# Kernel optimization log

Hardware: AMD Instinct MI355X
Metric: run time of the kernel (lower is better)

## Reference

```python
import jax, jax.numpy as jnp
import numpy as np
from jax import lax

# norse default LIF/LI parameters
DT = 0.001
TAU_SYN_INV = 200.0   # 1/5e-3
TAU_MEM_INV = 100.0   # 1/1e-2
V_TH = 1.0
ALPHA = 100.0         # super-spike surrogate slope
SEQ_LEN = 128         # args.sqlen
SCALE = 50.0          # args.scale
HIDDEN = 2048         # args.h2
STATE_DIM = 8         # LunarLander-v2
OUT = 4
BATCH = 256

@jax.custom_vjp
def superspike(x):
    # heaviside forward, SuperSpike surrogate backward
    return (x > 0).astype(x.dtype)

def _ss_fwd(x):
    return superspike(x), x

def _ss_bwd(x, g):
    return (g / (ALPHA * jnp.abs(x) + 1.0) ** 2,)

superspike.defvjp(_ss_fwd, _ss_bwd)

def constant_current_lif_encode(current):
    # current: [B, D]; returns spikes [T, B, D]
    def step(v, _):
        v = v + DT * TAU_MEM_INV * (current - v)  # v_leak = 0
        z = superspike(v - V_TH)
        v = (1.0 - z) * v                          # reset to 0
        return v, z
    _, zs = lax.scan(step, jnp.zeros_like(current), None, length=SEQ_LEN)
    return zs

def setup_inputs() -> dict:
    key = jax.random.key(0)
    k1, k2, k3, k4 = jax.random.split(key, 4)
    x = jax.random.normal(k1, (BATCH, STATE_DIM), dtype=jnp.float32)
    w_in = jax.random.normal(k2, (HIDDEN, 2 * STATE_DIM), dtype=jnp.float32) / np.sqrt(2 * STATE_DIM)
    w_rec = jax.random.normal(k3, (HIDDEN, HIDDEN), dtype=jnp.float32) / np.sqrt(HIDDEN)
    w_out = jax.random.normal(k4, (OUT, HIDDEN), dtype=jnp.float32) / np.sqrt(HIDDEN)
    return {"x": x, "w_in": w_in, "w_rec": w_rec, "w_out": w_out}

def reference(x, w_in, w_rec, w_out):
    # encode positive and negative rectified currents, concat on feature dim
    x_pos = constant_current_lif_encode(jax.nn.relu(SCALE * x))
    x_neg = constant_current_lif_encode(jax.nn.relu(-SCALE * x))
    xs = jnp.concatenate([x_pos, x_neg], axis=2)   # [T, B, 2*D]
    B = x.shape[0]
    H = w_in.shape[0]
    O = w_out.shape[0]
    # precompute feed-forward input currents for all timesteps (batched GEMM)
    cur_in = jnp.einsum('tbi,hi->tbh', xs, w_in)   # [T, B, H]
    def step(carry, c_t):
        z, v, i, vo, io = carry
        # LIF recurrent cell (norse lif_step): decay with old state, spike, reset, then current jump
        v_dec = v + DT * TAU_MEM_INV * (-v + i)
        i_dec = i * (1.0 - DT * TAU_SYN_INV)
        z_new = superspike(v_dec - V_TH)
        v_new = (1.0 - z_new) * v_dec              # v_reset = 0
        i_new = i_dec + c_t + z @ w_rec.T          # recurrent uses previous spikes
        # dropout p=0 (eval) -> identity
        # LI readout (norse li_linear_step): vo updates from old io, then io decays + jumps
        vo_new = vo + DT * TAU_MEM_INV * (-vo + io)
        io_new = io * (1.0 - DT * TAU_SYN_INV) + z_new @ w_out.T
        return (z_new, v_new, i_new, vo_new, io_new), vo_new
    dt = x.dtype
    init = (jnp.zeros((B, H), dt), jnp.zeros((B, H), dt), jnp.zeros((B, H), dt),
            jnp.zeros((B, O), dt), jnp.zeros((B, O), dt))
    _, voltages = lax.scan(step, init, cur_in)     # [T, B, O]
    m = jnp.max(voltages, axis=0)
    return jax.nn.softmax(m, axis=1)
```

## Files before the change

### kernel.cpp

```cpp
#include <hip/hip_runtime.h>
#include <math.h>

#define NB 256
#define NH 2048
#define ND 8
#define NI 16
#define NT 128
#define NO 4
#define KK2 33
#define NTHR 512

typedef __attribute__((ext_vector_type(4))) int i32x4;
typedef __attribute__((ext_vector_type(2))) long i64x2;
typedef __attribute__((ext_vector_type(2))) unsigned u32x2;

#define SSTR     (128u*KK2*1024u)
#define OFF_W4   0u
#define SZ_W4    (4u*SSTR)
#define OFF_SC   (OFF_W4 + SZ_W4)
#define OFF_SCF  (OFF_SC + 8192u)
#define ZBUF_B   (16u*KK2*1024u)
#define OFF_ZB   (OFF_SCF + 8192u)
#define SZ_ZB    (2u*ZBUF_B)
#define OFF_XS   (OFF_ZB + SZ_ZB)
#define SZ_XS    ((unsigned)NT*NB*NI)
#define OFF_V    (OFF_XS + SZ_XS)
#define SZ_V     ((unsigned)NB*NH*4u)
#define OFF_I    (OFF_V + SZ_V)
#define OFF_PIO  (OFF_I + SZ_V)
#define SZ_PIO   (2u*NB*64u*NO*4u)
#define OFF_VIO  (OFF_PIO + SZ_PIO)

__global__ __launch_bounds__(512) void k_scale(const float* __restrict__ w_rec,
                                               const float* __restrict__ w_in,
                                               char* __restrict__ wsb) {
    const int gt = blockIdx.x * 512 + threadIdx.x;
    const int h = gt >> 6, lane = gt & 63;
    float m = 0.0f;
    for (int k = lane; k < NH; k += 64) m = fmaxf(m, fabsf(w_rec[h * NH + k]));
    if (lane < 16) m = fmaxf(m, fabsf(w_in[h * NI + lane]));
    #pragma unroll
    for (int d = 1; d < 64; d <<= 1) m = fmaxf(m, __shfl_xor(m, d, 64));
    if (lane == 0) {
        int e;
        frexpf(m, &e);
        int s = 30 - e;
        ((float*)(wsb + OFF_SCF))[h] = ldexpf(1.0f, s);
        ((float*)(wsb + OFF_SC))[h]  = ldexpf(1.0f, -s);
    }
}

__global__ __launch_bounds__(192) void k_pack(const float* __restrict__ w_rec,
                                              const float* __restrict__ w_in,
                                              char* __restrict__ wsb) {
    const int h = blockIdx.x, c = threadIdx.x;
    if (c >= 132) return;
    const float scale = ((const float*)(wsb + OFF_SCF))[h];
    const int k0 = c * 16;
    const int kk = k0 >> 6, q = (k0 >> 4) & 3;
    unsigned pk[4][4] = {{0u,0u,0u,0u},{0u,0u,0u,0u},{0u,0u,0u,0u},{0u,0u,0u,0u}};
    #pragma unroll
    for (int u = 0; u < 16; ++u) {
        int k = k0 + u;
        float wv = 0.0f;
        if (k < NH) wv = w_rec[h * NH + k];
        else if (k < NH + NI) wv = w_in[h * NI + (k - NH)];
        int wq = __float2int_rn(wv * scale);
        int b0_ = (wq << 24) >> 24;  int r = (wq - b0_) >> 8;
        int b1_ = (r << 24) >> 24;   r = (r - b1_) >> 8;
        int b2_ = (r << 24) >> 24;   int b3_ = (r - b2_) >> 8;
        int bs[4] = {b0_, b1_, b2_, b3_};
        #pragma unroll
        for (int sp = 0; sp < 4; ++sp)
            pk[sp][u >> 2] |= ((unsigned)(unsigned char)bs[sp]) << ((u & 3) * 8);
    }
    char* w4 = wsb + OFF_W4;
    unsigned base = (((unsigned)(h >> 4)) * KK2 + (unsigned)kk) * 1024u
                  + ((unsigned)q * 16u + (unsigned)(h & 15)) * 16u;
    #pragma unroll
    for (int sp = 0; sp < 4; ++sp)
        *(i32x4*)(w4 + (unsigned)sp * SSTR + base) = *(const i32x4*)pk[sp];
}

__global__ __launch_bounds__(256) void k_init(const float* __restrict__ x,
                                              char* __restrict__ wsb) {
    const int g = blockIdx.x * 256 + threadIdx.x;
    unsigned* zb32 = (unsigned*)(wsb + OFF_ZB);
    float* vst = (float*)(wsb + OFF_V);
    float* ist = (float*)(wsb + OFF_I);
    float* vio = (float*)(wsb + OFF_VIO);
    char* xsp = (char*)(wsb + OFF_XS);

    #pragma unroll
    for (int r = 0; r < 5; ++r) {
        unsigned off = (unsigned)g + (unsigned)r * 65536u;
        if (off < (SZ_ZB / 4u)) zb32[off] = 0u;
    }
    #pragma unroll
    for (int r = 0; r < 8; ++r) vst[g + r * 65536] = 0.0f;
    #pragma unroll
    for (int r = 0; r < 8; ++r) ist[g + r * 65536] = 0.0f;
    if (g < 3072) vio[g] = (g < 2048) ? 0.0f : -3.0e38f;

    if (g < NB * NI) {
        const int b = g >> 4, ci = g & 15;
        float xv = x[b * ND + (ci & 7)];
        float c = (ci < 8) ? __fmul_rn(50.0f, xv) : __fmul_rn(-50.0f, xv);
        c = fmaxf(c, 0.0f);
        float ev = 0.0f;
        for (int t = 0; t < NT; ++t) {
            ev = __fadd_rn(ev, __fmul_rn(0.1f, __fsub_rn(c, ev)));
            float z = (__fsub_rn(ev, 1.0f) > 0.0f) ? 1.0f : 0.0f;
            xsp[t * (NB * NI) + g] = (z > 0.0f) ? (char)1 : (char)0;
            ev = (z > 0.0f) ? 0.0f : ev;
        }
    }
}

__global__ __launch_bounds__(256) void k_init2(char* __restrict__ wsb) {
    const int b = threadIdx.x;
    char* zb0 = wsb + OFF_ZB;
    const char* xsp = wsb + OFF_XS;
    i32x4 xv = *(const i32x4*)(xsp + b * 16);
    unsigned dst = (((unsigned)(b >> 4)) * KK2 + 32u) * 1024u + (unsigned)(b & 15) * 16u;
    *(i32x4*)(zb0 + dst) = xv;
}

__global__ __launch_bounds__(NTHR, 2) void k_step(const float* __restrict__ w_out,
                                                  char* __restrict__ wsb, int t) {
    __shared__ float red[4 * 64 * 34];
    __shared__ float z_s[64 * 34];
    __shared__ float w_out_lds[128];

    const int tid = threadIdx.x;
    const int beta = blockIdx.x;
    const int xcd = beta & 7, jb = beta >> 3;
    const int ht = xcd * 8 + (jb & 7);
    const int bt = jb >> 3;
    const int b0 = bt * 64, h0 = ht * 32;

    const char* w4 = wsb + OFF_W4;
    const float* inv_scale = (const float*)(wsb + OFF_SC);
    char* zb = wsb + OFF_ZB;
    const char* xsp = wsb + OFF_XS;
    float* vst = (float*)(wsb + OFF_V);
    float* ist = (float*)(wsb + OFF_I);
    float* pio = (float*)(wsb + OFF_PIO);
    float* vio = (float*)(wsb + OFF_VIO);

    const char* zr = zb + (t & 1) * ZBUF_B;
    char* zw = zb + ((t + 1) & 1) * ZBUF_B;

    const int g = beta * NTHR + tid;
    if (t > 0 && g < NB * NO) {
        const float* pr = pio + ((t - 1) & 1) * (NB * 64 * NO);
        const int b = g >> 2, o = g & 3;
        float s = 0.0f;
        #pragma unroll
        for (int jj = 0; jj < 64; ++jj) s += pr[(b * 64 + jj) * NO + o];
        float vo = vio[g], io = vio[1024 + g], mx = vio[2048 + g];
        float von = __fadd_rn(vo, __fmul_rn(0.1f, __fsub_rn(io, vo)));
        io = __fadd_rn(__fmul_rn(io, 0.8f), s);
        vio[g] = von; vio[1024 + g] = io; vio[2048 + g] = fmaxf(mx, von);
    }

    if (ht == 0 && t + 1 < NT && tid < 64) {
        int bg = b0 + tid;
        i32x4 xv = *(const i32x4*)(xsp + ((t + 1) * NB + bg) * 16);
        unsigned dst = (((unsigned)(bg >> 4)) * KK2 + 32u) * 1024u
                     + (unsigned)(bg & 15) * 16u;
        *(i32x4*)(zw + dst) = xv;
    }
    if (tid < 128) w_out_lds[tid] = w_out[(tid >> 5) * NH + h0 + (tid & 31)];

    const int w = tid >> 6, lane = tid & 63;
    const unsigned h16a = (unsigned)(ht * 2);

    i32x4 acc[4][2][4];
    #pragma unroll
    for (int rb = 0; rb < 4; ++rb)
        #pragma unroll
        for (int hb = 0; hb < 2; ++hb)
            #pragma unroll
            for (int sp = 0; sp < 4; ++sp) acc[rb][hb][sp] = (i32x4){0, 0, 0, 0};

    for (int kk = w; kk < KK2; kk += 8) {
        i64x2 a[4];
        #pragma unroll
        for (int rb = 0; rb < 4; ++rb) {
            unsigned off = (((unsigned)(bt * 4 + rb)) * KK2 + (unsigned)kk) * 1024u
                         + (unsigned)lane * 16u;
            a[rb] = *(const i64x2*)(zr + off);
        }
        #pragma unroll
        for (int sp = 0; sp < 4; ++sp) {
            #pragma unroll
            for (int hb = 0; hb < 2; ++hb) {
                unsigned off = (unsigned)sp * SSTR
                             + ((h16a + (unsigned)hb) * KK2 + (unsigned)kk) * 1024u
                             + (unsigned)lane * 16u;
                i64x2 bfr = *(const i64x2*)(w4 + off);
                #pragma unroll
                for (int rb = 0; rb < 4; ++rb) {
                    acc[rb][hb][sp] = __builtin_amdgcn_mfma_i32_16x16x32_i8(
                        a[rb][0], bfr[0], acc[rb][hb][sp], 0, 0, 0);
                    acc[rb][hb][sp] = __builtin_amdgcn_mfma_i32_16x16x32_i8(
                        a[rb][1], bfr[1], acc[rb][hb][sp], 0, 0, 0);
                }
            }
        }
    }

    const int lk = lane >> 4, lh = lane & 15;
    const float inv0 = inv_scale[h0 + lh], inv1 = inv_scale[h0 + 16 + lh];
    float fc[4][2][4];
    #pragma unroll
    for (int rb = 0; rb < 4; ++rb)
        #pragma unroll
        for (int hb = 0; hb < 2; ++hb) {
            float invs = hb ? inv1 : inv0;
            #pragma unroll
            for (int r = 0; r < 4; ++r) {
                float f = fmaf((float)acc[rb][hb][3][r], 16777216.0f,
                          fmaf((float)acc[rb][hb][2][r], 65536.0f,
                          fmaf((float)acc[rb][hb][1][r], 256.0f,
                               (float)acc[rb][hb][0][r])));
                fc[rb][hb][r] = f * invs;
            }
        }
    if (w >= 4) {
        #pragma unroll
        for (int rb = 0; rb < 4; ++rb)
            #pragma unroll
            for (int hb = 0; hb < 2; ++hb)
                #pragma unroll
                for (int r = 0; r < 4; ++r)
                    red[(w - 4) * 2176 + (rb * 16 + lk * 4 + r) * 34 + hb * 16 + lh]
                        = fc[rb][hb][r];
    }
    __syncthreads();
    if (w < 4) {
        #pragma unroll
        for (int rb = 0; rb < 4; ++rb)
            #pragma unroll
            for (int hb = 0; hb < 2; ++hb)
                #pragma unroll
                for (int r = 0; r < 4; ++r) {
                    int ro = w * 2176 + (rb * 16 + lk * 4 + r) * 34 + hb * 16 + lh;
                    red[ro] = fc[rb][hb][r] + red[ro];
                }
    }
    __syncthreads();

    #pragma unroll
    for (int e = 0; e < 4; ++e) {
        int idx = e * NTHR + tid;
        int bl = idx >> 5, hl = idx & 31;
        int ro = bl * 34 + hl;
        float accv = ((red[ro] + red[2176 + ro]) + red[2 * 2176 + ro]) + red[3 * 2176 + ro];
        int gidx = (b0 + bl) * NH + h0 + hl;
        float vv = vst[gidx], ii = ist[gidx];
        float vd = __fadd_rn(vv, __fmul_rn(0.1f, __fsub_rn(ii, vv)));
        float zn = (__fsub_rn(vd, 1.0f) > 0.0f) ? 1.0f : 0.0f;
        vst[gidx] = (zn > 0.0f) ? 0.0f : vd;
        ist[gidx] = __fadd_rn(__fmul_rn(ii, 0.8f), accv);
        z_s[ro] = zn;
    }
    __syncthreads();

    if (tid < 256) {
        int b = tid >> 2, c = tid & 3;
        int bg = b0 + b;
        unsigned lo_u = 0, hi_u = 0;
        #pragma unroll
        for (int jj = 0; jj < 4; ++jj)
            lo_u |= (z_s[b * 34 + c * 8 + jj] > 0.5f ? 1u : 0u) << (jj * 8);
        #pragma unroll
        for (int jj = 0; jj < 4; ++jj)
            hi_u |= (z_s[b * 34 + c * 8 + 4 + jj] > 0.5f ? 1u : 0u) << (jj * 8);
        unsigned q = (unsigned)((ht & 1) * 2 + (c >> 1));
        unsigned dst = (((unsigned)(bg >> 4)) * KK2 + (unsigned)(ht >> 1)) * 1024u
                     + (q * 16u + (unsigned)(bg & 15)) * 16u + (unsigned)((c & 1) * 8);
        *(u32x2*)(zw + dst) = (u32x2){lo_u, hi_u};

        int o = tid & 3;
        float s = 0.0f;
        #pragma unroll
        for (int h = 0; h < 32; ++h)
            s = fmaf(z_s[b * 34 + h], w_out_lds[o * 32 + h], s);
        float* pw = pio + (t & 1) * (NB * 64 * NO);
        pw[((b0 + b) * 64 + ht) * NO + o] = s;
    }
}

__global__ __launch_bounds__(256) void k_final(char* __restrict__ wsb,
                                               float* __restrict__ out) {
    const int g = blockIdx.x * 256 + threadIdx.x;
    if (g >= NB * NO) return;
    float* vio = (float*)(wsb + OFF_VIO);
    float vo = vio[g], io = vio[1024 + g], mx = vio[2048 + g];
    float von = __fadd_rn(vo, __fmul_rn(0.1f, __fsub_rn(io, vo)));
    mx = fmaxf(mx, von);

    float mm = fmaxf(mx, __shfl_xor(mx, 1, 64));
    mm = fmaxf(mm, __shfl_xor(mm, 2, 64));
    float e = expf(__fsub_rn(mx, mm));
    float es = e;
    es += __shfl_xor(es, 1, 64);
    es += __shfl_xor(es, 2, 64);
    out[g] = e / es;
}

extern "C" void kernel_launch(void* const* d_in, const int* in_sizes, int n_in,
                              void* d_out, int out_size, void* d_ws, size_t ws_size,
                              hipStream_t stream) {
    const float* x     = (const float*)d_in[0];
    const float* w_in  = (const float*)d_in[1];
    const float* w_rec = (const float*)d_in[2];
    const float* w_out = (const float*)d_in[3];
    float* out = (float*)d_out;
    char* wsb  = (char*)d_ws;

    k_scale<<<256, 512, 0, stream>>>(w_rec, w_in, wsb);
    k_pack<<<NH, 192, 0, stream>>>(w_rec, w_in, wsb);
    k_init<<<256, 256, 0, stream>>>(x, wsb);
    k_init2<<<1, 256, 0, stream>>>(wsb);
    for (int t = 0; t < NT; ++t)
        k_step<<<256, NTHR, 0, stream>>>(w_out, wsb, t);
    k_final<<<4, 256, 0, stream>>>(wsb, out);
}
```

Measured before the change: 1.678 ms.

## Use 3-slice int8 weight split and 1024-thread blocks in recurrent step

Weights are now quantized to about 23 bits and split into three int8 slices instead of four, which cuts MFMA work and weight-read traffic per step by a quarter. The step kernel doubles its block size to 1024 threads. Each wave now covers two row blocks instead of four, so its register accumulator footprint shrinks. The output readout update is moved into block 0 alone. The lower precision could change spike decisions near threshold, and the occupancy bound is raised to 4.

After: 1.983 ms. 1.18x slower.

```diff
diff --git a/kernel.cpp b/kernel.cpp
--- a/kernel.cpp
+++ b/kernel.cpp
@@ -8,16 +8,16 @@
 #define NT 128
 #define NO 4
 #define KK2 33
-#define NTHR 512
+#define NTHR 1024
 
 typedef __attribute__((ext_vector_type(4))) int i32x4;
 typedef __attribute__((ext_vector_type(2))) long i64x2;
 typedef __attribute__((ext_vector_type(2))) unsigned u32x2;
 
 #define SSTR     (128u*KK2*1024u)
-#define OFF_W4   0u
-#define SZ_W4    (4u*SSTR)
-#define OFF_SC   (OFF_W4 + SZ_W4)
+#define OFF_W3   0u
+#define SZ_W3    (3u*SSTR)
+#define OFF_SC   (OFF_W3 + SZ_W3)
 #define OFF_SCF  (OFF_SC + 8192u)
 #define ZBUF_B   (16u*KK2*1024u)
 #define OFF_ZB   (OFF_SCF + 8192u)
@@ -44,7 +44,7 @@
     if (lane == 0) {
         int e;
         frexpf(m, &e);
-        int s = 30 - e;
+        int s = 22 - e;
         ((float*)(wsb + OFF_SCF))[h] = ldexpf(1.0f, s);
         ((float*)(wsb + OFF_SC))[h]  = ldexpf(1.0f, -s);
     }
@@ -58,7 +58,7 @@
     const float scale = ((const float*)(wsb + OFF_SCF))[h];
     const int k0 = c * 16;
     const int kk = k0 >> 6, q = (k0 >> 4) & 3;
-    unsigned pk[4][4] = {{0u,0u,0u,0u},{0u,0u,0u,0u},{0u,0u,0u,0u},{0u,0u,0u,0u}};
+    unsigned pk[3][4] = {{0u,0u,0u,0u},{0u,0u,0u,0u},{0u,0u,0u,0u}};
     #pragma unroll
     for (int u = 0; u < 16; ++u) {
         int k = k0 + u;
@@ -67,19 +67,18 @@
         else if (k < NH + NI) wv = w_in[h * NI + (k - NH)];
         int wq = __float2int_rn(wv * scale);
         int b0_ = (wq << 24) >> 24;  int r = (wq - b0_) >> 8;
-        int b1_ = (r << 24) >> 24;   r = (r - b1_) >> 8;
-        int b2_ = (r << 24) >> 24;   int b3_ = (r - b2_) >> 8;
-        int bs[4] = {b0_, b1_, b2_, b3_};
-        #pragma unroll
-        for (int sp = 0; sp < 4; ++sp)
+        int b1_ = (r << 24) >> 24;   int b2_ = (r - b1_) >> 8;
+        int bs[3] = {b0_, b1_, b2_};
+        #pragma unroll
+        for (int sp = 0; sp < 3; ++sp)
             pk[sp][u >> 2] |= ((unsigned)(unsigned char)bs[sp]) << ((u & 3) * 8);
     }
-    char* w4 = wsb + OFF_W4;
+    char* w3 = wsb + OFF_W3;
     unsigned base = (((unsigned)(h >> 4)) * KK2 + (unsigned)kk) * 1024u
                   + ((unsigned)q * 16u + (unsigned)(h & 15)) * 16u;
     #pragma unroll
-    for (int sp = 0; sp < 4; ++sp)
-        *(i32x4*)(w4 + (unsigned)sp * SSTR + base) = *(const i32x4*)pk[sp];
+    for (int sp = 0; sp < 3; ++sp)
+        *(i32x4*)(w3 + (unsigned)sp * SSTR + base) = *(const i32x4*)pk[sp];
 }
 
 __global__ __launch_bounds__(256) void k_init(const float* __restrict__ x,
@@ -126,7 +125,7 @@
     *(i32x4*)(zb0 + dst) = xv;
 }
 
-__global__ __launch_bounds__(NTHR, 2) void k_step(const float* __restrict__ w_out,
+__global__ __launch_bounds__(NTHR, 4) void k_step(const float* __restrict__ w_out,
                                                   char* __restrict__ wsb, int t) {
     __shared__ float red[4 * 64 * 34];
     __shared__ float z_s[64 * 34];
@@ -139,7 +138,7 @@
     const int bt = jb >> 3;
     const int b0 = bt * 64, h0 = ht * 32;
 
-    const char* w4 = wsb + OFF_W4;
+    const char* w3 = wsb + OFF_W3;
     const float* inv_scale = (const float*)(wsb + OFF_SC);
     char* zb = wsb + OFF_ZB;
     const char* xsp = wsb + OFF_XS;
@@ -151,17 +150,16 @@
     const char* zr = zb + (t & 1) * ZBUF_B;
     char* zw = zb + ((t + 1) & 1) * ZBUF_B;
 
-    const int g = beta * NTHR + tid;
-    if (t > 0 && g < NB * NO) {
+    if (t > 0 && beta == 0) {
         const float* pr = pio + ((t - 1) & 1) * (NB * 64 * NO);
-        const int b = g >> 2, o = g & 3;
+        const int b = tid >> 2, o = tid & 3;
         float s = 0.0f;
         #pragma unroll
         for (int jj = 0; jj < 64; ++jj) s += pr[(b * 64 + jj) * NO + o];
-        float vo = vio[g], io = vio[1024 + g], mx = vio[2048 + g];
+        float vo = vio[tid], io = vio[1024 + tid], mx = vio[2048 + tid];
         float von = __fadd_rn(vo, __fmul_rn(0.1f, __fsub_rn(io, vo)));
         io = __fadd_rn(__fmul_rn(io, 0.8f), s);
-        vio[g] = von; vio[1024 + g] = io; vio[2048 + g] = fmaxf(mx, von);
+        vio[tid] = von; vio[1024 + tid] = io; vio[2048 + tid] = fmaxf(mx, von);
     }
 
     if (ht == 0 && t + 1 < NT && tid < 64) {
@@ -174,86 +172,89 @@
     if (tid < 128) w_out_lds[tid] = w_out[(tid >> 5) * NH + h0 + (tid & 31)];
 
     const int w = tid >> 6, lane = tid & 63;
+    const int kw = w & 7, rbg = w >> 3;
     const unsigned h16a = (unsigned)(ht * 2);
 
-    i32x4 acc[4][2][4];
-    #pragma unroll
-    for (int rb = 0; rb < 4; ++rb)
+    i32x4 acc[2][2][3];
+    #pragma unroll
+    for (int rb = 0; rb < 2; ++rb)
         #pragma unroll
         for (int hb = 0; hb < 2; ++hb)
             #pragma unroll
-            for (int sp = 0; sp < 4; ++sp) acc[rb][hb][sp] = (i32x4){0, 0, 0, 0};
-
-    for (int kk = w; kk < KK2; kk += 8) {
-        i64x2 a[4];
-        #pragma unroll
-        for (int rb = 0; rb < 4; ++rb) {
-            unsigned off = (((unsigned)(bt * 4 + rb)) * KK2 + (unsigned)kk) * 1024u
-                         + (unsigned)lane * 16u;
-            a[rb] = *(const i64x2*)(zr + off);
-        }
-        #pragma unroll
-        for (int sp = 0; sp < 4; ++sp) {
+            for (int sp = 0; sp < 3; ++sp) acc[rb][hb][sp] = (i32x4){0, 0, 0, 0};
+
+    const char* zA0 = zr + ((unsigned)(bt * 4 + rbg * 2) * KK2) * 1024u
+                    + (unsigned)lane * 16u;
+    const char* zA1 = zA0 + (unsigned)KK2 * 1024u;
+    const char* wB  = w3 + (h16a * KK2) * 1024u + (unsigned)lane * 16u;
+    const unsigned hstr = (unsigned)KK2 * 1024u;
+
+    for (int kk = kw; kk < KK2; kk += 8) {
+        const unsigned o = (unsigned)kk * 1024u;
+        i64x2 a0 = *(const i64x2*)(zA0 + o);
+        i64x2 a1 = *(const i64x2*)(zA1 + o);
+        #pragma unroll
+        for (int sp = 0; sp < 3; ++sp) {
             #pragma unroll
             for (int hb = 0; hb < 2; ++hb) {
-                unsigned off = (unsigned)sp * SSTR
-                             + ((h16a + (unsigned)hb) * KK2 + (unsigned)kk) * 1024u
-                             + (unsigned)lane * 16u;
-                i64x2 bfr = *(const i64x2*)(w4 + off);
-                #pragma unroll
-                for (int rb = 0; rb < 4; ++rb) {
-                    acc[rb][hb][sp] = __builtin_amdgcn_mfma_i32_16x16x32_i8(
-                        a[rb][0], bfr[0], acc[rb][hb][sp], 0, 0, 0);
-                    acc[rb][hb][sp] = __builtin_amdgcn_mfma_i32_16x16x32_i8(
-                        a[rb][1], bfr[1], acc[rb][hb][sp], 0, 0, 0);
-                }
+                i64x2 bfr = *(const i64x2*)(wB + (unsigned)sp * SSTR
+                                               + (unsigned)hb * hstr + o);
+                acc[0][hb][sp] = __builtin_amdgcn_mfma_i32_16x16x32_i8(
+                    a0[0], bfr[0], acc[0][hb][sp], 0, 0, 0);
+                acc[0][hb][sp] = __builtin_amdgcn_mfma_i32_16x16x32_i8(
+                    a0[1], bfr[1], acc[0][hb][sp], 0, 0, 0);
+                acc[1][hb][sp] = __builtin_amdgcn_mfma_i32_16x16x32_i8(
+                    a1[0], bfr[0], acc[1][hb][sp], 0, 0, 0);
+                acc[1][hb][sp] = __builtin_amdgcn_mfma_i32_16x16x32_i8(
+                    a1[1], bfr[1], acc[1][hb][sp], 0, 0, 0);
             }
         }
     }
 
     const int lk = lane >> 4, lh = lane & 15;
     const float inv0 = inv_scale[h0 + lh], inv1 = inv_scale[h0 + 16 + lh];
-    float fc[4][2][4];
-    #pragma unroll
-    for (int rb = 0; rb < 4; ++rb)
+    float fc[2][2][4];
+    #pragma unroll
+    for (int rb = 0; rb < 2; ++rb)
         #pragma unroll
         for (int hb = 0; hb < 2; ++hb) {
             float invs = hb ? inv1 : inv0;
             #pragma unroll
             for (int r = 0; r < 4; ++r) {
-                float f = fmaf((float)acc[rb][hb][3][r], 16777216.0f,
-                          fmaf((float)acc[rb][hb][2][r], 65536.0f,
+                float f = fmaf((float)acc[rb][hb][2][r], 65536.0f,
                           fmaf((float)acc[rb][hb][1][r], 256.0f,
-                               (float)acc[rb][hb][0][r])));
+                               (float)acc[rb][hb][0][r]));
                 fc[rb][hb][r] = f * invs;
             }
         }
-    if (w >= 4) {
-        #pragma unroll
-        for (int rb = 0; rb < 4; ++rb)
+    if (kw >= 4) {
+        #pragma unroll
+        for (int rb = 0; rb < 2; ++rb)
             #pragma unroll
             for (int hb = 0; hb < 2; ++hb)
                 #pragma unroll
                 for (int r = 0; r < 4; ++r)
-                    red[(w - 4) * 2176 + (rb * 16 + lk * 4 + r) * 34 + hb * 16 + lh]
+                    red[(kw - 4) * 2176
+                        + (rbg * 32 + rb * 16 + lk * 4 + r) * 34 + hb * 16 + lh]
                         = fc[rb][hb][r];
     }
     __syncthreads();
-    if (w < 4) {
-        #pragma unroll
-        for (int rb = 0; rb < 4; ++rb)
+    if (kw < 4) {
+        #pragma unroll
+        for (int rb = 0; rb < 2; ++rb)
             #pragma unroll
             for (int hb = 0; hb < 2; ++hb)
                 #pragma unroll
                 for (int r = 0; r < 4; ++r) {
-                    int ro = w * 2176 + (rb * 16 + lk * 4 + r) * 34 + hb * 16 + lh;
+                    int ro = kw * 2176
+                           + (rbg * 32 + rb * 16 + lk * 4 + r) * 34 + hb * 16 + lh;
                     red[ro] = fc[rb][hb][r] + red[ro];
                 }
     }
     __syncthreads();
 
     #pragma unroll
-    for (int e = 0; e < 4; ++e) {
+    for (int e = 0; e < 2; ++e) {
         int idx = e * NTHR + tid;
         int bl = idx >> 5, hl = idx & 31;
         int ro = bl * 34 + hl;
```

## Split input projection out of int8 K loop and double-buffer MFMA operand loads

Applied to the files above, without the earlier changes.

The 16 input-feature columns are removed from the quantized int8 recurrent GEMM, which cuts K from 33 to 32 chunks so each of the 8 waves handles exactly 4. The input current is now computed in fp32 inside the step kernel from LDS-staged spikes and w_in. The K loop is fully unrolled with double-buffered register loads of A and B fragments to overlap global loads with MFMAs. This drops the k_init2 launch and the per-step uneven-wave tail. It adds LDS usage and a small per-element 16-term FMA, and changes how the input term is rounded relative to the quantized path.

Result: slower. 1.849 ms (+10.2%).

```diff
diff --git a/kernel.cpp b/kernel.cpp
--- a/kernel.cpp
+++ b/kernel.cpp
@@ -7,19 +7,19 @@
 #define NI 16
 #define NT 128
 #define NO 4
-#define KK2 33
+#define KK 32
 #define NTHR 512
 
 typedef __attribute__((ext_vector_type(4))) int i32x4;
 typedef __attribute__((ext_vector_type(2))) long i64x2;
 typedef __attribute__((ext_vector_type(2))) unsigned u32x2;
 
-#define SSTR     (128u*KK2*1024u)
+#define SSTR     (128u*KK*1024u)
 #define OFF_W4   0u
 #define SZ_W4    (4u*SSTR)
 #define OFF_SC   (OFF_W4 + SZ_W4)
 #define OFF_SCF  (OFF_SC + 8192u)
-#define ZBUF_B   (16u*KK2*1024u)
+#define ZBUF_B   (16u*KK*1024u)
 #define OFF_ZB   (OFF_SCF + 8192u)
 #define SZ_ZB    (2u*ZBUF_B)
 #define OFF_XS   (OFF_ZB + SZ_ZB)
@@ -32,13 +32,11 @@
 #define OFF_VIO  (OFF_PIO + SZ_PIO)
 
 __global__ __launch_bounds__(512) void k_scale(const float* __restrict__ w_rec,
-                                               const float* __restrict__ w_in,
                                                char* __restrict__ wsb) {
     const int gt = blockIdx.x * 512 + threadIdx.x;
     const int h = gt >> 6, lane = gt & 63;
     float m = 0.0f;
     for (int k = lane; k < NH; k += 64) m = fmaxf(m, fabsf(w_rec[h * NH + k]));
-    if (lane < 16) m = fmaxf(m, fabsf(w_in[h * NI + lane]));
     #pragma unroll
     for (int d = 1; d < 64; d <<= 1) m = fmaxf(m, __shfl_xor(m, d, 64));
     if (lane == 0) {
@@ -50,21 +48,16 @@
     }
 }
 
-__global__ __launch_bounds__(192) void k_pack(const float* __restrict__ w_rec,
-                                              const float* __restrict__ w_in,
+__global__ __launch_bounds__(128) void k_pack(const float* __restrict__ w_rec,
                                               char* __restrict__ wsb) {
     const int h = blockIdx.x, c = threadIdx.x;
-    if (c >= 132) return;
     const float scale = ((const float*)(wsb + OFF_SCF))[h];
     const int k0 = c * 16;
     const int kk = k0 >> 6, q = (k0 >> 4) & 3;
     unsigned pk[4][4] = {{0u,0u,0u,0u},{0u,0u,0u,0u},{0u,0u,0u,0u},{0u,0u,0u,0u}};
     #pragma unroll
     for (int u = 0; u < 16; ++u) {
-        int k = k0 + u;
-        float wv = 0.0f;
-        if (k < NH) wv = w_rec[h * NH + k];
-        else if (k < NH + NI) wv = w_in[h * NI + (k - NH)];
+        float wv = w_rec[h * NH + k0 + u];
         int wq = __float2int_rn(wv * scale);
         int b0_ = (wq << 24) >> 24;  int r = (wq - b0_) >> 8;
         int b1_ = (r << 24) >> 24;   r = (r - b1_) >> 8;
@@ -75,7 +68,7 @@
             pk[sp][u >> 2] |= ((unsigned)(unsigned char)bs[sp]) << ((u & 3) * 8);
     }
     char* w4 = wsb + OFF_W4;
-    unsigned base = (((unsigned)(h >> 4)) * KK2 + (unsigned)kk) * 1024u
+    unsigned base = (((unsigned)(h >> 4)) * KK + (unsigned)kk) * 1024u
                   + ((unsigned)q * 16u + (unsigned)(h & 15)) * 16u;
     #pragma unroll
     for (int sp = 0; sp < 4; ++sp)
@@ -92,10 +85,7 @@
     char* xsp = (char*)(wsb + OFF_XS);
 
     #pragma unroll
-    for (int r = 0; r < 5; ++r) {
-        unsigned off = (unsigned)g + (unsigned)r * 65536u;
-        if (off < (SZ_ZB / 4u)) zb32[off] = 0u;
-    }
+    for (int r = 0; r < 4; ++r) zb32[g + r * 65536] = 0u;
     #pragma unroll
     for (int r = 0; r < 8; ++r) vst[g + r * 65536] = 0.0f;
     #pragma unroll
@@ -117,19 +107,13 @@
     }
 }
 
-__global__ __launch_bounds__(256) void k_init2(char* __restrict__ wsb) {
-    const int b = threadIdx.x;
-    char* zb0 = wsb + OFF_ZB;
-    const char* xsp = wsb + OFF_XS;
-    i32x4 xv = *(const i32x4*)(xsp + b * 16);
-    unsigned dst = (((unsigned)(b >> 4)) * KK2 + 32u) * 1024u + (unsigned)(b & 15) * 16u;
-    *(i32x4*)(zb0 + dst) = xv;
-}
-
-__global__ __launch_bounds__(NTHR, 2) void k_step(const float* __restrict__ w_out,
+__global__ __launch_bounds__(NTHR, 2) void k_step(const float* __restrict__ w_in,
+                                                  const float* __restrict__ w_out,
                                                   char* __restrict__ wsb, int t) {
     __shared__ float red[4 * 64 * 34];
     __shared__ float z_s[64 * 34];
+    __shared__ float xs_f[64 * 17];
+    __shared__ float w_in_lds[32 * 17];
     __shared__ float w_out_lds[128];
 
     const int tid = threadIdx.x;
@@ -164,17 +148,22 @@
         vio[g] = von; vio[1024 + g] = io; vio[2048 + g] = fmaxf(mx, von);
     }
 
-    if (ht == 0 && t + 1 < NT && tid < 64) {
-        int bg = b0 + tid;
-        i32x4 xv = *(const i32x4*)(xsp + ((t + 1) * NB + bg) * 16);
-        unsigned dst = (((unsigned)(bg >> 4)) * KK2 + 32u) * 1024u
-                     + (unsigned)(bg & 15) * 16u;
-        *(i32x4*)(zw + dst) = xv;
+    #pragma unroll
+    for (int r = 0; r < 2; ++r) {
+        int v = tid + r * NTHR;
+        int bl = v >> 4, ci = v & 15;
+        xs_f[bl * 17 + ci] = (float)xsp[t * (NB * NI) + (b0 + bl) * NI + ci];
+    }
+    {
+        int hl = tid >> 4, i2 = tid & 15;
+        w_in_lds[hl * 17 + i2] = w_in[(h0 + hl) * NI + i2];
     }
     if (tid < 128) w_out_lds[tid] = w_out[(tid >> 5) * NH + h0 + (tid & 31)];
 
     const int w = tid >> 6, lane = tid & 63;
     const unsigned h16a = (unsigned)(ht * 2);
+    const unsigned lb = (unsigned)lane * 16u;
+    const unsigned kk0 = (unsigned)(w * 4);
 
     i32x4 acc[4][2][4];
     #pragma unroll
@@ -184,31 +173,45 @@
             #pragma unroll
             for (int sp = 0; sp < 4; ++sp) acc[rb][hb][sp] = (i32x4){0, 0, 0, 0};
 
-    for (int kk = w; kk < KK2; kk += 8) {
-        i64x2 a[4];
-        #pragma unroll
-        for (int rb = 0; rb < 4; ++rb) {
-            unsigned off = (((unsigned)(bt * 4 + rb)) * KK2 + (unsigned)kk) * 1024u
-                         + (unsigned)lane * 16u;
-            a[rb] = *(const i64x2*)(zr + off);
+    const char* zA = zr + (((unsigned)(bt * 4) * KK + kk0) * 1024u) + lb;
+    const char* wB = w4 + ((h16a * KK + kk0) * 1024u) + lb;
+
+    i64x2 a[2][4], bv[2][2][4];
+    #pragma unroll
+    for (int rb = 0; rb < 4; ++rb)
+        a[0][rb] = *(const i64x2*)(zA + (unsigned)rb * 32768u);
+    #pragma unroll
+    for (int hb = 0; hb < 2; ++hb)
+        #pragma unroll
+        for (int sp = 0; sp < 4; ++sp)
+            bv[0][hb][sp] = *(const i64x2*)(wB + (unsigned)sp * SSTR + (unsigned)hb * 32768u);
+
+    #pragma unroll
+    for (int c = 0; c < 4; ++c) {
+        const int cur = c & 1, nxt = cur ^ 1;
+        if (c < 3) {
+            const unsigned co = (unsigned)(c + 1) * 1024u;
+            #pragma unroll
+            for (int rb = 0; rb < 4; ++rb)
+                a[nxt][rb] = *(const i64x2*)(zA + (unsigned)rb * 32768u + co);
+            #pragma unroll
+            for (int hb = 0; hb < 2; ++hb)
+                #pragma unroll
+                for (int sp = 0; sp < 4; ++sp)
+                    bv[nxt][hb][sp] = *(const i64x2*)(wB + (unsigned)sp * SSTR
+                                                         + (unsigned)hb * 32768u + co);
         }
         #pragma unroll
-        for (int sp = 0; sp < 4; ++sp) {
-            #pragma unroll
-            for (int hb = 0; hb < 2; ++hb) {
-                unsigned off = (unsigned)sp * SSTR
-                             + ((h16a + (unsigned)hb) * KK2 + (unsigned)kk) * 1024u
-                             + (unsigned)lane * 16u;
-                i64x2 bfr = *(const i64x2*)(w4 + off);
+        for (int sp = 0; sp < 4; ++sp)
+            #pragma unroll
+            for (int hb = 0; hb < 2; ++hb)
                 #pragma unroll
                 for (int rb = 0; rb < 4; ++rb) {
                     acc[rb][hb][sp] = __builtin_amdgcn_mfma_i32_16x16x32_i8(
-                        a[rb][0], bfr[0], acc[rb][hb][sp], 0, 0, 0);
+                        a[cur][rb][0], bv[cur][hb][sp][0], acc[rb][hb][sp], 0, 0, 0);
                     acc[rb][hb][sp] = __builtin_amdgcn_mfma_i32_16x16x32_i8(
-                        a[rb][1], bfr[1], acc[rb][hb][sp], 0, 0, 0);
+                        a[cur][rb][1], bv[cur][hb][sp][1], acc[rb][hb][sp], 0, 0, 0);
                 }
-            }
-        }
     }
 
     const int lk = lane >> 4, lh = lane & 15;
@@ -258,12 +261,16 @@
         int bl = idx >> 5, hl = idx & 31;
         int ro = bl * 34 + hl;
         float accv = ((red[ro] + red[2176 + ro]) + red[2 * 2176 + ro]) + red[3 * 2176 + ro];
+        float c = 0.0f;
+        #pragma unroll
+        for (int i = 0; i < NI; ++i)
+            c = fmaf(xs_f[bl * 17 + i], w_in_lds[hl * 17 + i], c);
         int gidx = (b0 + bl) * NH + h0 + hl;
         float vv = vst[gidx], ii = ist[gidx];
         float vd = __fadd_rn(vv, __fmul_rn(0.1f, __fsub_rn(ii, vv)));
         float zn = (__fsub_rn(vd, 1.0f) > 0.0f) ? 1.0f : 0.0f;
         vst[gidx] = (zn > 0.0f) ? 0.0f : vd;
-        ist[gidx] = __fadd_rn(__fmul_rn(ii, 0.8f), accv);
+        ist[gidx] = __fadd_rn(__fadd_rn(__fmul_rn(ii, 0.8f), c), accv);
         z_s[ro] = zn;
     }
     __syncthreads();
@@ -279,7 +286,7 @@
         for (int jj = 0; jj < 4; ++jj)
             hi_u |= (z_s[b * 34 + c * 8 + 4 + jj] > 0.5f ? 1u : 0u) << (jj * 8);
         unsigned q = (unsigned)((ht & 1) * 2 + (c >> 1));
-        unsigned dst = (((unsigned)(bg >> 4)) * KK2 + (unsigned)(ht >> 1)) * 1024u
+        unsigned dst = (((unsigned)(bg >> 4)) * KK + (unsigned)(ht >> 1)) * 1024u
                      + (q * 16u + (unsigned)(bg & 15)) * 16u + (unsigned)((c & 1) * 8);
         *(u32x2*)(zw + dst) = (u32x2){lo_u, hi_u};
 
@@ -321,11 +328,10 @@
     float* out = (float*)d_out;
     char* wsb  = (char*)d_ws;
 
-    k_scale<<<256, 512, 0, stream>>>(w_rec, w_in, wsb);
-    k_pack<<<NH, 192, 0, stream>>>(w_rec, w_in, wsb);
+    k_scale<<<256, 512, 0, stream>>>(w_rec, wsb);
+    k_pack<<<NH, 128, 0, stream>>>(w_rec, wsb);
     k_init<<<256, 256, 0, stream>>>(x, wsb);
-    k_init2<<<1, 256, 0, stream>>>(wsb);
     for (int t = 0; t < NT; ++t)
-        k_step<<<256, NTHR, 0, stream>>>(w_out, wsb, t);
+        k_step<<<256, NTHR, 0, stream>>>(w_in, w_out, wsb, t);
     k_final<<<4, 256, 0, stream>>>(wsb, out);
 }
```

## Halve per-block batch tile to 32 rows and launch 512 step blocks

Applied to the files above, without the earlier changes.

Each per-timestep block now covers 32 batch rows instead of 64, so the grid doubles to 512 blocks. Accumulators and LDS reduction buffers shrink, and launch bounds now allow 4 blocks per CU. The aim is to spread the latency-bound recurrent int8 MFMA step over more CUs and waves. In exchange, each weight tile is loaded twice as often across blocks. The spike packing and w_out partial-sum code is reworked to fit the new tile shape.

After: 1.618 ms. 1.04x faster.

```diff
diff --git a/kernel.cpp b/kernel.cpp
--- a/kernel.cpp
+++ b/kernel.cpp
@@ -7,19 +7,19 @@
 #define NI 16
 #define NT 128
 #define NO 4
-#define KK2 33
+#define KKT 33
 #define NTHR 512
+#define NBLK 512
 
 typedef __attribute__((ext_vector_type(4))) int i32x4;
 typedef __attribute__((ext_vector_type(2))) long i64x2;
-typedef __attribute__((ext_vector_type(2))) unsigned u32x2;
-
-#define SSTR     (128u*KK2*1024u)
+
+#define SSTR     (128u*KKT*1024u)
 #define OFF_W4   0u
 #define SZ_W4    (4u*SSTR)
 #define OFF_SC   (OFF_W4 + SZ_W4)
 #define OFF_SCF  (OFF_SC + 8192u)
-#define ZBUF_B   (16u*KK2*1024u)
+#define ZBUF_B   (16u*KKT*1024u)
 #define OFF_ZB   (OFF_SCF + 8192u)
 #define SZ_ZB    (2u*ZBUF_B)
 #define OFF_XS   (OFF_ZB + SZ_ZB)
@@ -28,8 +28,8 @@
 #define SZ_V     ((unsigned)NB*NH*4u)
 #define OFF_I    (OFF_V + SZ_V)
 #define OFF_PIO  (OFF_I + SZ_V)
-#define SZ_PIO   (2u*NB*64u*NO*4u)
-#define OFF_VIO  (OFF_PIO + SZ_PIO)
+#define PIOHALF  (NB*64*NO)
+#define OFF_VIO  (OFF_PIO + 2u*PIOHALF*4u)
 
 __global__ __launch_bounds__(512) void k_scale(const float* __restrict__ w_rec,
                                                const float* __restrict__ w_in,
@@ -75,7 +75,7 @@
             pk[sp][u >> 2] |= ((unsigned)(unsigned char)bs[sp]) << ((u & 3) * 8);
     }
     char* w4 = wsb + OFF_W4;
-    unsigned base = (((unsigned)(h >> 4)) * KK2 + (unsigned)kk) * 1024u
+    unsigned base = (((unsigned)(h >> 4)) * KKT + (unsigned)kk) * 1024u
                   + ((unsigned)q * 16u + (unsigned)(h & 15)) * 16u;
     #pragma unroll
     for (int sp = 0; sp < 4; ++sp)
@@ -122,22 +122,22 @@
     char* zb0 = wsb + OFF_ZB;
     const char* xsp = wsb + OFF_XS;
     i32x4 xv = *(const i32x4*)(xsp + b * 16);
-    unsigned dst = (((unsigned)(b >> 4)) * KK2 + 32u) * 1024u + (unsigned)(b & 15) * 16u;
-    *(i32x4*)(zb0 + dst) = xv;
-}
-
-__global__ __launch_bounds__(NTHR, 2) void k_step(const float* __restrict__ w_out,
+    *(i32x4*)(zb0 + (((unsigned)(b >> 4)) * KKT + 32u) * 1024u
+                  + (unsigned)(b & 15) * 16u) = xv;
+}
+
+__global__ __launch_bounds__(NTHR, 4) void k_step(const float* __restrict__ w_out,
                                                   char* __restrict__ wsb, int t) {
-    __shared__ float red[4 * 64 * 34];
-    __shared__ float z_s[64 * 34];
+    __shared__ float red[4][32 * 33];
+    __shared__ float z_s[32 * 33];
     __shared__ float w_out_lds[128];
 
     const int tid = threadIdx.x;
-    const int beta = blockIdx.x;
-    const int xcd = beta & 7, jb = beta >> 3;
-    const int ht = xcd * 8 + (jb & 7);
-    const int bt = jb >> 3;
-    const int b0 = bt * 64, h0 = ht * 32;
+    const int blk = blockIdx.x;
+    const int xcd = blk & 7, j = blk >> 3;
+    const int ht = xcd * 8 + (j & 7);
+    const int bt = j >> 3;
+    const int b0 = bt * 32, h0 = ht * 32;
 
     const char* w4 = wsb + OFF_W4;
     const float* inv_scale = (const float*)(wsb + OFF_SC);
@@ -151,71 +151,69 @@
     const char* zr = zb + (t & 1) * ZBUF_B;
     char* zw = zb + ((t + 1) & 1) * ZBUF_B;
 
-    const int g = beta * NTHR + tid;
+    const int g = blk * NTHR + tid;
     if (t > 0 && g < NB * NO) {
-        const float* pr = pio + ((t - 1) & 1) * (NB * 64 * NO);
+        const float* pr = pio + ((t - 1) & 1) * PIOHALF;
         const int b = g >> 2, o = g & 3;
         float s = 0.0f;
         #pragma unroll
-        for (int jj = 0; jj < 64; ++jj) s += pr[(b * 64 + jj) * NO + o];
+        for (int jj = 0; jj < 64; ++jj) s += pr[b * 256 + jj * 4 + o];
         float vo = vio[g], io = vio[1024 + g], mx = vio[2048 + g];
         float von = __fadd_rn(vo, __fmul_rn(0.1f, __fsub_rn(io, vo)));
         io = __fadd_rn(__fmul_rn(io, 0.8f), s);
         vio[g] = von; vio[1024 + g] = io; vio[2048 + g] = fmaxf(mx, von);
     }
 
-    if (ht == 0 && t + 1 < NT && tid < 64) {
-        int bg = b0 + tid;
+    if (ht == 8 && t + 1 < NT && tid < 32) {
+        const int bg = b0 + tid;
         i32x4 xv = *(const i32x4*)(xsp + ((t + 1) * NB + bg) * 16);
-        unsigned dst = (((unsigned)(bg >> 4)) * KK2 + 32u) * 1024u
-                     + (unsigned)(bg & 15) * 16u;
-        *(i32x4*)(zw + dst) = xv;
+        *(i32x4*)(zw + (((unsigned)(bg >> 4)) * KKT + 32u) * 1024u
+                     + (unsigned)(bg & 15) * 16u) = xv;
     }
     if (tid < 128) w_out_lds[tid] = w_out[(tid >> 5) * NH + h0 + (tid & 31)];
 
     const int w = tid >> 6, lane = tid & 63;
-    const unsigned h16a = (unsigned)(ht * 2);
-
-    i32x4 acc[4][2][4];
-    #pragma unroll
-    for (int rb = 0; rb < 4; ++rb)
+    const unsigned lane16 = (unsigned)lane * 16u;
+
+    i32x4 acc[2][2][4];
+    #pragma unroll
+    for (int rb = 0; rb < 2; ++rb)
         #pragma unroll
         for (int hb = 0; hb < 2; ++hb)
             #pragma unroll
             for (int sp = 0; sp < 4; ++sp) acc[rb][hb][sp] = (i32x4){0, 0, 0, 0};
 
-    for (int kk = w; kk < KK2; kk += 8) {
-        i64x2 a[4];
-        #pragma unroll
-        for (int rb = 0; rb < 4; ++rb) {
-            unsigned off = (((unsigned)(bt * 4 + rb)) * KK2 + (unsigned)kk) * 1024u
-                         + (unsigned)lane * 16u;
-            a[rb] = *(const i64x2*)(zr + off);
-        }
+    const char* zA = zr + ((unsigned)(bt * 2) * KKT) * 1024u + lane16;
+    const char* wB = w4 + ((unsigned)(ht * 2) * KKT) * 1024u + lane16;
+    const unsigned rstr = (unsigned)KKT * 1024u;
+
+    for (int kk = w; kk < KKT; kk += 8) {
+        const unsigned o = (unsigned)kk * 1024u;
+        i64x2 a0 = *(const i64x2*)(zA + o);
+        i64x2 a1 = *(const i64x2*)(zA + rstr + o);
         #pragma unroll
         for (int sp = 0; sp < 4; ++sp) {
             #pragma unroll
             for (int hb = 0; hb < 2; ++hb) {
-                unsigned off = (unsigned)sp * SSTR
-                             + ((h16a + (unsigned)hb) * KK2 + (unsigned)kk) * 1024u
-                             + (unsigned)lane * 16u;
-                i64x2 bfr = *(const i64x2*)(w4 + off);
-                #pragma unroll
-                for (int rb = 0; rb < 4; ++rb) {
-                    acc[rb][hb][sp] = __builtin_amdgcn_mfma_i32_16x16x32_i8(
-                        a[rb][0], bfr[0], acc[rb][hb][sp], 0, 0, 0);
-                    acc[rb][hb][sp] = __builtin_amdgcn_mfma_i32_16x16x32_i8(
-                        a[rb][1], bfr[1], acc[rb][hb][sp], 0, 0, 0);
-                }
+                i64x2 bf = *(const i64x2*)(wB + (unsigned)sp * SSTR
+                                              + (unsigned)hb * rstr + o);
+                acc[0][hb][sp] = __builtin_amdgcn_mfma_i32_16x16x32_i8(
+                    a0[0], bf[0], acc[0][hb][sp], 0, 0, 0);
+                acc[0][hb][sp] = __builtin_amdgcn_mfma_i32_16x16x32_i8(
+                    a0[1], bf[1], acc[0][hb][sp], 0, 0, 0);
+                acc[1][hb][sp] = __builtin_amdgcn_mfma_i32_16x16x32_i8(
+                    a1[0], bf[0], acc[1][hb][sp], 0, 0, 0);
+                acc[1][hb][sp] = __builtin_amdgcn_mfma_i32_16x16x32_i8(
+                    a1[1], bf[1], acc[1][hb][sp], 0, 0, 0);
             }
         }
     }
 
     const int lk = lane >> 4, lh = lane & 15;
     const float inv0 = inv_scale[h0 + lh], inv1 = inv_scale[h0 + 16 + lh];
-    float fc[4][2][4];
-    #pragma unroll
-    for (int rb = 0; rb < 4; ++rb)
+    float fc[2][2][4];
+    #pragma unroll
+    for (int rb = 0; rb < 2; ++rb)
         #pragma unroll
         for (int hb = 0; hb < 2; ++hb) {
             float invs = hb ? inv1 : inv0;
@@ -230,34 +228,34 @@
         }
     if (w >= 4) {
         #pragma unroll
-        for (int rb = 0; rb < 4; ++rb)
+        for (int rb = 0; rb < 2; ++rb)
             #pragma unroll
             for (int hb = 0; hb < 2; ++hb)
                 #pragma unroll
                 for (int r = 0; r < 4; ++r)
-                    red[(w - 4) * 2176 + (rb * 16 + lk * 4 + r) * 34 + hb * 16 + lh]
+                    red[w - 4][(rb * 16 + lk * 4 + r) * 33 + hb * 16 + lh]
                         = fc[rb][hb][r];
     }
     __syncthreads();
     if (w < 4) {
         #pragma unroll
-        for (int rb = 0; rb < 4; ++rb)
+        for (int rb = 0; rb < 2; ++rb)
             #pragma unroll
             for (int hb = 0; hb < 2; ++hb)
                 #pragma unroll
                 for (int r = 0; r < 4; ++r) {
-                    int ro = w * 2176 + (rb * 16 + lk * 4 + r) * 34 + hb * 16 + lh;
-                    red[ro] = fc[rb][hb][r] + red[ro];
+                    int ro = (rb * 16 + lk * 4 + r) * 33 + hb * 16 + lh;
+                    red[w][ro] = fc[rb][hb][r] + red[w][ro];
                 }
     }
     __syncthreads();
 
     #pragma unroll
-    for (int e = 0; e < 4; ++e) {
+    for (int e = 0; e < 2; ++e) {
         int idx = e * NTHR + tid;
         int bl = idx >> 5, hl = idx & 31;
-        int ro = bl * 34 + hl;
-        float accv = ((red[ro] + red[2176 + ro]) + red[2 * 2176 + ro]) + red[3 * 2176 + ro];
+        int ro = bl * 33 + hl;
+        float accv = ((red[0][ro] + red[1][ro]) + red[2][ro]) + red[3][ro];
         int gidx = (b0 + bl) * NH + h0 + hl;
         float vv = vst[gidx], ii = ist[gidx];
         float vd = __fadd_rn(vv, __fmul_rn(0.1f, __fsub_rn(ii, vv)));
@@ -269,27 +267,25 @@
     __syncthreads();
 
     if (tid < 256) {
-        int b = tid >> 2, c = tid & 3;
-        int bg = b0 + b;
-        unsigned lo_u = 0, hi_u = 0;
+        const int b = tid >> 3, seg = tid & 7;
+        const int bg = b0 + b;
+        unsigned uw = 0;
         #pragma unroll
         for (int jj = 0; jj < 4; ++jj)
-            lo_u |= (z_s[b * 34 + c * 8 + jj] > 0.5f ? 1u : 0u) << (jj * 8);
-        #pragma unroll
-        for (int jj = 0; jj < 4; ++jj)
-            hi_u |= (z_s[b * 34 + c * 8 + 4 + jj] > 0.5f ? 1u : 0u) << (jj * 8);
-        unsigned q = (unsigned)((ht & 1) * 2 + (c >> 1));
-        unsigned dst = (((unsigned)(bg >> 4)) * KK2 + (unsigned)(ht >> 1)) * 1024u
-                     + (q * 16u + (unsigned)(bg & 15)) * 16u + (unsigned)((c & 1) * 8);
-        *(u32x2*)(zw + dst) = (u32x2){lo_u, hi_u};
-
-        int o = tid & 3;
+            uw |= (z_s[b * 33 + seg * 4 + jj] > 0.5f ? 1u : 0u) << (jj * 8);
+        const unsigned q = (unsigned)((ht & 1) * 2 + (seg >> 2));
+        *(unsigned*)(zw + (((unsigned)(bg >> 4)) * KKT + (unsigned)(ht >> 1)) * 1024u
+                        + (q * 16u + (unsigned)(bg & 15)) * 16u + (unsigned)((seg & 3) * 4))
+            = uw;
+    }
+    if (tid < 128) {
+        const int b = tid >> 2, o = tid & 3;
         float s = 0.0f;
         #pragma unroll
         for (int h = 0; h < 32; ++h)
-            s = fmaf(z_s[b * 34 + h], w_out_lds[o * 32 + h], s);
-        float* pw = pio + (t & 1) * (NB * 64 * NO);
-        pw[((b0 + b) * 64 + ht) * NO + o] = s;
+            s = fmaf(z_s[b * 33 + h], w_out_lds[o * 32 + h], s);
+        float* pw = pio + (t & 1) * PIOHALF;
+        pw[(b0 + b) * 256 + ht * 4 + o] = s;
     }
 }
 
@@ -326,6 +322,6 @@
     k_init<<<256, 256, 0, stream>>>(x, wsb);
     k_init2<<<1, 256, 0, stream>>>(wsb);
     for (int t = 0; t < NT; ++t)
-        k_step<<<256, NTHR, 0, stream>>>(w_out, wsb, t);
+        k_step<<<NBLK, NTHR, 0, stream>>>(w_out, wsb, t);
     k_final<<<4, 256, 0, stream>>>(wsb, out);
 }
```
